# Kernel optimization log

Hardware: AMD Instinct MI355X
Metric: run time of the kernel (lower is better)

The kernel has to match this reference:

```python
import jax, jax.numpy as jnp
import numpy as np

D = 128      # internal_dimensions
L = 4        # num_edge_convs
N = 100000   # nodes
E = 800000   # edges
G = 64       # graphs
IN = 4       # in_channels


def _ln(x, g, b):
    m = jnp.mean(x, -1, keepdims=True)
    v = jnp.mean((x - m) ** 2, -1, keepdims=True)
    return (x - m) * jax.lax.rsqrt(v + 1e-5) * g + b


def _gelu(x):
    return jax.nn.gelu(x, approximate=False)  # torch nn.GELU default (erf)


def _seg_mean(x, seg, n):
    s = jax.ops.segment_sum(x, seg, num_segments=n)
    c = jax.ops.segment_sum(jnp.ones((x.shape[0], 1), x.dtype), seg, num_segments=n)
    return s / jnp.maximum(c, 1.0)


def _seg_max(x, seg, n):
    m = jax.ops.segment_max(x, seg, num_segments=n)
    return jnp.where(jnp.isfinite(m), m, 0.0)  # empty segments -> 0 (PyG convention)


def _forward(x, edge_index, batch, num_graphs,
             in_W1, in_b1, in_g1, in_bn1, in_W2, in_b2, in_g2, in_bn2,
             pre_g, pre_b, cW1, cb1, cg1, cbb1, cW2, cb2, cg2, cbb2, pW, pb,
             ag_g, ag_b,
             kW1, kb1, kg1, kbb1, kW2, kb2, kg2, kbb2,
             kW3, kb3, kg3, kbb3, kW4, kb4):
    n = x.shape[0]
    # input_net: Linear -> LN -> GELU -> Linear -> LN   (dropout=0, eval)
    h = _gelu(_ln(x @ in_W1 + in_b1, in_g1, in_bn1))
    h = _ln(h @ in_W2 + in_b2, in_g2, in_bn2)

    x_in_max = _seg_max(h, batch, num_graphs)
    x_in_mean = _seg_mean(h, batch, num_graphs)

    src, dst = edge_index[0], edge_index[1]  # PyG: message from src (x_j) to dst (x_i)
    xcur = h
    for l in range(L):
        identity = xcur
        hn = _ln(xcur, pre_g[l], pre_b[l])
        xi = hn[dst]            # [E, D]
        xj = hn[src]            # [E, D]
        m = jnp.concatenate([xi, xj - xi], axis=-1)       # [E, 2D]
        m = _gelu(_ln(m @ cW1[l] + cb1[l], cg1[l], cbb1[l]))
        m = _gelu(_ln(m @ cW2[l] + cb2[l], cg2[l], cbb2[l]))
        a_max = _seg_max(m, dst, n)
        a_mean = _seg_mean(m, dst, n)
        aggr = jnp.concatenate([a_max, a_mean], axis=-1)  # [N, 2D]
        xcur = identity + aggr @ pW[l] + pb[l]

    xcur = _ln(xcur, ag_g, ag_b)
    x_g_max = _seg_max(xcur, batch, num_graphs)
    x_g_mean = _seg_mean(xcur, batch, num_graphs)

    xp = jnp.concatenate([x_in_max, x_in_mean, x_g_max, x_g_mean], axis=-1)  # [G, 4D]
    z = _gelu(_ln(xp @ kW1 + kb1, kg1, kbb1))
    z = _gelu(_ln(z @ kW2 + kb2, kg2, kbb2))
    z = _gelu(_ln(z @ kW3 + kb3, kg3, kbb3))
    return z @ kW4 + kb4  # [G, 1]


def setup_inputs() -> dict:
    key = jax.random.key(0)
    ks = iter(jax.random.split(key, 64))
    def W(shape, fan):
        return jax.random.normal(next(ks), shape, jnp.float32) * np.float32((2.0 / fan) ** 0.5)
    inp = {}
    inp["x"] = jax.random.normal(next(ks), (N, IN), jnp.float32)
    inp["edge_index"] = jax.random.randint(next(ks), (2, E), 0, N)
    inp["batch"] = jnp.sort(jax.random.randint(next(ks), (N,), 0, G))
    inp["num_graphs"] = G
    inp["in_W1"] = W((IN, D), IN); inp["in_b1"] = jnp.zeros((D,), jnp.float32)
    inp["in_g1"] = jnp.ones((D,), jnp.float32); inp["in_bn1"] = jnp.zeros((D,), jnp.float32)
    inp["in_W2"] = W((D, D), D); inp["in_b2"] = jnp.zeros((D,), jnp.float32)
    inp["in_g2"] = jnp.ones((D,), jnp.float32); inp["in_bn2"] = jnp.zeros((D,), jnp.float32)
    inp["pre_g"] = jnp.ones((L, D), jnp.float32); inp["pre_b"] = jnp.zeros((L, D), jnp.float32)
    inp["cW1"] = W((L, 2 * D, D), 2 * D); inp["cb1"] = jnp.zeros((L, D), jnp.float32)
    inp["cg1"] = jnp.ones((L, D), jnp.float32); inp["cbb1"] = jnp.zeros((L, D), jnp.float32)
    inp["cW2"] = W((L, D, D), D); inp["cb2"] = jnp.zeros((L, D), jnp.float32)
    inp["cg2"] = jnp.ones((L, D), jnp.float32); inp["cbb2"] = jnp.zeros((L, D), jnp.float32)
    inp["pW"] = W((L, 2 * D, D), 2 * D); inp["pb"] = jnp.zeros((L, D), jnp.float32)
    inp["ag_g"] = jnp.ones((D,), jnp.float32); inp["ag_b"] = jnp.zeros((D,), jnp.float32)
    inp["kW1"] = W((4 * D, D), 4 * D); inp["kb1"] = jnp.zeros((D,), jnp.float32)
    inp["kg1"] = jnp.ones((D,), jnp.float32); inp["kbb1"] = jnp.zeros((D,), jnp.float32)
    inp["kW2"] = W((D, D), D); inp["kb2"] = jnp.zeros((D,), jnp.float32)
    inp["kg2"] = jnp.ones((D,), jnp.float32); inp["kbb2"] = jnp.zeros((D,), jnp.float32)
    inp["kW3"] = W((D, D // 4), D); inp["kb3"] = jnp.zeros((D // 4,), jnp.float32)
    inp["kg3"] = jnp.ones((D // 4,), jnp.float32); inp["kbb3"] = jnp.zeros((D // 4,), jnp.float32)
    inp["kW4"] = W((D // 4, 1), D // 4); inp["kb4"] = jnp.zeros((1,), jnp.float32)
    return inp


def reference(x, edge_index, batch, num_graphs,
              in_W1, in_b1, in_g1, in_bn1, in_W2, in_b2, in_g2, in_bn2,
              pre_g, pre_b, cW1, cb1, cg1, cbb1, cW2, cb2, cg2, cbb2, pW, pb,
              ag_g, ag_b,
              kW1, kb1, kg1, kbb1, kW2, kb2, kg2, kbb2,
              kW3, kb3, kg3, kbb3, kW4, kb4):
    return _forward(x, edge_index, batch, num_graphs,
                    in_W1, in_b1, in_g1, in_bn1, in_W2, in_b2, in_g2, in_bn2,
                    pre_g, pre_b, cW1, cb1, cg1, cbb1, cW2, cb2, cg2, cbb2, pW, pb,
                    ag_g, ag_b,
                    kW1, kb1, kg1, kbb1, kW2, kb2, kg2, kbb2,
                    kW3, kb3, kg3, kbb3, kW4, kb4)
```

## Files before the change

### kernel.cpp

```cpp
#include <hip/hip_runtime.h>
#include <hip/hip_bf16.h>
#include <math.h>

__device__ __forceinline__ float geluf(float x) {
    return 0.5f * x * (1.0f + erff(x * 0.70710678118654752f));
}
#define MAPNEGINF 0x007FFFFFu
__device__ __forceinline__ float funmap(unsigned m) {
    return __uint_as_float((m & 0x80000000u) ? (m ^ 0x80000000u) : ~m);
}
__device__ __forceinline__ unsigned fmap(float f) {
    unsigned u = __float_as_uint(f);
    return ((int)u < 0) ? ~u : (u | 0x80000000u);
}
__device__ __forceinline__ float wred64(float v) {
#pragma unroll
    for (int m = 1; m < 64; m <<= 1) v += __shfl_xor(v, m);
    return v;
}
__device__ __forceinline__ unsigned short bf16r(float f) {
    unsigned u = __float_as_uint(f);
    u += 0x7fffu + ((u >> 16) & 1u);
    return (unsigned short)(u >> 16);
}

__device__ __forceinline__ void stage_wq(float* Ws, const float* __restrict__ src, int t) {
#pragma unroll
    for (int it = 0; it < 4; ++it) {
        const int idx = it * 1024 + (t << 2);
        *(float4*)(Ws + idx) = *(const float4*)(src + idx);
    }
}

__device__ __forceinline__ void kloop_q(const float* As, const float* Ws, float (&acc)[4][8],
                                        const int r0, const int ogc, const int kb) {
#pragma unroll
    for (int kk = 0; kk < 32; kk += 4) {
        const float4 a0 = *(const float4*)(As + (r0 + 0) * 132 + kb + kk);
        const float4 a1 = *(const float4*)(As + (r0 + 1) * 132 + kb + kk);
        const float4 a2 = *(const float4*)(As + (r0 + 2) * 132 + kb + kk);
        const float4 a3 = *(const float4*)(As + (r0 + 3) * 132 + kb + kk);
#define MAD8(R, AV)                                                                     \
    {                                                                                   \
        acc[R][0] += (AV)*wA.x; acc[R][1] += (AV)*wA.y; acc[R][2] += (AV)*wA.z;         \
        acc[R][3] += (AV)*wA.w; acc[R][4] += (AV)*wB.x; acc[R][5] += (AV)*wB.y;         \
        acc[R][6] += (AV)*wB.z; acc[R][7] += (AV)*wB.w;                                 \
    }
#define KSTEP(J, C)                                                                     \
    {                                                                                   \
        const float4 wA = *(const float4*)(Ws + (kk + (J)) * 128 + ogc);                \
        const float4 wB = *(const float4*)(Ws + (kk + (J)) * 128 + 64 + ogc);           \
        MAD8(0, a0.C) MAD8(1, a1.C) MAD8(2, a2.C) MAD8(3, a3.C)                         \
    }
        KSTEP(0, x) KSTEP(1, y) KSTEP(2, z) KSTEP(3, w)
#undef KSTEP
#undef MAD8
    }
}

__global__ void k_zero(unsigned* __restrict__ p, int n) {
    const int i = blockIdx.x * 256 + threadIdx.x;
    if (i < n) p[i] = 0u;
}

__global__ void k_copyu(const unsigned* __restrict__ a, const unsigned* __restrict__ b,
                        unsigned* __restrict__ ac, unsigned* __restrict__ bc, int n) {
    const int i = blockIdx.x * 256 + threadIdx.x;
    if (i < n) {
        ac[i] = a[i];
        bc[i] = b[i];
    }
}

__global__ void k_count(const int* __restrict__ ei, unsigned* __restrict__ deg, int E) {
    const int e = blockIdx.x * 256 + threadIdx.x;
    if (e < E) atomicAdd(deg + ei[E + e], 1u);
}

__global__ void k_scan1(const unsigned* __restrict__ deg, unsigned* __restrict__ excl,
                        unsigned* __restrict__ bsum, int n) {
    __shared__ unsigned sh[256];
    const int t = threadIdx.x;
    const int base = blockIdx.x * 1024 + t * 4;
    unsigned v0 = (base + 0 < n) ? deg[base + 0] : 0u;
    unsigned v1 = (base + 1 < n) ? deg[base + 1] : 0u;
    unsigned v2 = (base + 2 < n) ? deg[base + 2] : 0u;
    unsigned v3 = (base + 3 < n) ? deg[base + 3] : 0u;
    const unsigned s = v0 + v1 + v2 + v3;
    sh[t] = s;
    __syncthreads();
    for (int off = 1; off < 256; off <<= 1) {
        unsigned x = 0;
        if (t >= off) x = sh[t - off];
        __syncthreads();
        if (t >= off) sh[t] += x;
        __syncthreads();
    }
    const unsigned ebase = sh[t] - s;
    if (base + 0 < n) excl[base + 0] = ebase;
    if (base + 1 < n) excl[base + 1] = ebase + v0;
    if (base + 2 < n) excl[base + 2] = ebase + v0 + v1;
    if (base + 3 < n) excl[base + 3] = ebase + v0 + v1 + v2;
    if (t == 255) bsum[blockIdx.x] = sh[255];
}

__global__ void k_scan2(unsigned* __restrict__ bsum, int nb) {
    __shared__ unsigned sh[256];
    const int t = threadIdx.x;
    const unsigned v = (t < nb) ? bsum[t] : 0u;
    sh[t] = v;
    __syncthreads();
    for (int off = 1; off < 256; off <<= 1) {
        unsigned x = 0;
        if (t >= off) x = sh[t - off];
        __syncthreads();
        if (t >= off) sh[t] += x;
        __syncthreads();
    }
    if (t < nb) bsum[t] = sh[t] - v;
}

__global__ void k_scan3(unsigned* __restrict__ excl, const unsigned* __restrict__ bsum, int n) {
    const int t = threadIdx.x;
    const int base = blockIdx.x * 1024 + t * 4;
    const unsigned add = bsum[blockIdx.x];
#pragma unroll
    for (int j = 0; j < 4; ++j)
        if (base + j < n) excl[base + j] += add;
}

__global__ void k_scatter(const int* __restrict__ ei, unsigned* __restrict__ cursor,
                          int* __restrict__ esrc, int* __restrict__ edst, int E) {
    const int e = blockIdx.x * 256 + threadIdx.x;
    if (e < E) {
        const int s = ei[e];
        const int d = ei[E + e];
        const unsigned pos = atomicAdd(cursor + d, 1u);
        esrc[pos] = s;
        edst[pos] = d;
    }
}

__global__ void k_in1(const float* __restrict__ x, const float* __restrict__ W1,
                      const float* __restrict__ b1, const float* __restrict__ g1,
                      const float* __restrict__ bn1, float* __restrict__ h, int n) {
    const int t = threadIdx.x, lane = t & 63, wave = t >> 6;
    const int d0 = lane << 1;
    const float2 w0 = *(const float2*)(W1 + d0);
    const float2 w1 = *(const float2*)(W1 + 128 + d0);
    const float2 w2 = *(const float2*)(W1 + 256 + d0);
    const float2 w3 = *(const float2*)(W1 + 384 + d0);
    const float2 bb = *(const float2*)(b1 + d0);
    const float2 gg = *(const float2*)(g1 + d0);
    const float2 nn = *(const float2*)(bn1 + d0);
    const int stride = gridDim.x * 4;
    for (int node = blockIdx.x * 4 + wave; node < n; node += stride) {
        const float4 xv = *(const float4*)(x + (size_t)node * 4);
        float h0 = bb.x + xv.x * w0.x + xv.y * w1.x + xv.z * w2.x + xv.w * w3.x;
        float h1 = bb.y + xv.x * w0.y + xv.y * w1.y + xv.z * w2.y + xv.w * w3.y;
        const float s = wred64(h0 + h1), q = wred64(h0 * h0 + h1 * h1);
        const float mean = s * 0.0078125f, var = q * 0.0078125f - mean * mean;
        const float rs = rsqrtf(var + 1e-5f);
        h0 = geluf((h0 - mean) * rs * gg.x + nn.x);
        h1 = geluf((h1 - mean) * rs * gg.y + nn.y);
        *(float2*)(h + (size_t)node * 128 + d0) = make_float2(h0, h1);
    }
}

__global__ __launch_bounds__(256, 2) void k_in2(const float* __restrict__ A,
                                                const float* __restrict__ W,
                                                const float* __restrict__ bias,
                                                const float* __restrict__ g,
                                                const float* __restrict__ b,
                                                float* __restrict__ C, int n) {
    __shared__ float As[64 * 132];
    __shared__ float Ws[4096];
    const int t = threadIdx.x;
    const int n0 = blockIdx.x * 64;
    {
        const int r = t >> 2, c0 = (t & 3) << 5;
        const int row = n0 + r;
        const bool ok = row < n;
#pragma unroll
        for (int j = 0; j < 8; ++j) {
            const int col = c0 + (j << 2);
            float4 v = make_float4(0.f, 0.f, 0.f, 0.f);
            if (ok) v = *(const float4*)(A + (size_t)row * 128 + col);
            *(float4*)(As + r * 132 + col) = v;
        }
    }
    float acc[4][8];
#pragma unroll
    for (int r = 0; r < 4; ++r)
#pragma unroll
        for (int o = 0; o < 8; ++o) acc[r][o] = 0.f;
    const int og = t & 15, eg = t >> 4;
    const int ogc = og << 2, r0 = eg << 2;
#pragma unroll
    for (int q4 = 0; q4 < 4; ++q4) {
        stage_wq(Ws, W + q4 * 4096, t);
        __syncthreads();
        kloop_q(As, Ws, acc, r0, ogc, q4 * 32);
        __syncthreads();
    }
    const float4 bA = *(const float4*)(bias + ogc);
    const float4 bB = *(const float4*)(bias + 64 + ogc);
    const float4 gA = *(const float4*)(g + ogc);
    const float4 gB = *(const float4*)(g + 64 + ogc);
    const float4 lA = *(const float4*)(b + ogc);
    const float4 lB = *(const float4*)(b + 64 + ogc);
#pragma unroll
    for (int r = 0; r < 4; ++r) {
        float v[8];
        v[0] = acc[r][0] + bA.x; v[1] = acc[r][1] + bA.y;
        v[2] = acc[r][2] + bA.z; v[3] = acc[r][3] + bA.w;
        v[4] = acc[r][4] + bB.x; v[5] = acc[r][5] + bB.y;
        v[6] = acc[r][6] + bB.z; v[7] = acc[r][7] + bB.w;
        float s = 0.f, q = 0.f;
#pragma unroll
        for (int o = 0; o < 8; ++o) { s += v[o]; q += v[o] * v[o]; }
#pragma unroll
        for (int m = 1; m < 16; m <<= 1) { s += __shfl_xor(s, m); q += __shfl_xor(q, m); }
        const float mean = s * 0.0078125f;
        const float var = q * 0.0078125f - mean * mean;
        const float rs = rsqrtf(var + 1e-5f);
        const int row = n0 + r0 + r;
        if (row < n) {
            *(float4*)(C + (size_t)row * 128 + ogc) = make_float4(
                (v[0] - mean) * rs * gA.x + lA.x, (v[1] - mean) * rs * gA.y + lA.y,
                (v[2] - mean) * rs * gA.z + lA.z, (v[3] - mean) * rs * gA.w + lA.w);
            *(float4*)(C + (size_t)row * 128 + 64 + ogc) = make_float4(
                (v[4] - mean) * rs * gB.x + lB.x, (v[5] - mean) * rs * gB.y + lB.y,
                (v[6] - mean) * rs * gB.z + lB.z, (v[7] - mean) * rs * gB.w + lB.w);
        }
    }
}

__global__ void k_ln(const float* __restrict__ in, const float* __restrict__ g,
                     const float* __restrict__ b, float* __restrict__ out, int n) {
    const int t = threadIdx.x, lane = t & 63, wave = t >> 6;
    const int d0 = lane << 1;
    const float ga = g[d0], gb = g[d0 + 1], ba = b[d0], bb = b[d0 + 1];
    const int stride = gridDim.x * 4;
    for (int node = blockIdx.x * 4 + wave; node < n; node += stride) {
        const float2 v = *(const float2*)(in + (size_t)node * 128 + d0);
        const float s = wred64(v.x + v.y), q = wred64(v.x * v.x + v.y * v.y);
        const float mean = s * 0.0078125f, var = q * 0.0078125f - mean * mean;
        const float rs = rsqrtf(var + 1e-5f);
        *(float2*)(out + (size_t)node * 128 + d0) =
            make_float2((v.x - mean) * rs * ga + ba, (v.y - mean) * rs * gb + bb);
    }
}

__global__ void k_wxj(const float* __restrict__ c, float* __restrict__ Wx,
                      float* __restrict__ Wj) {
    const int idx = blockIdx.x * 256 + threadIdx.x;
    const float a = c[idx], b = c[16384 + idx];
    Wx[idx] = a - b;
    Wj[idx] = b;
}

__global__ __launch_bounds__(256, 2) void k_gemmh(const float* __restrict__ A,
                                                  const float* __restrict__ W,
                                                  const float* __restrict__ bias,
                                                  unsigned short* __restrict__ C, int n) {
    __shared__ float As[64 * 132];
    __shared__ float Ws[4096];
    const int t = threadIdx.x;
    const int n0 = blockIdx.x * 64;
    {
        const int r = t >> 2, c0 = (t & 3) << 5;
        const int row = n0 + r;
        const bool ok = row < n;
#pragma unroll
        for (int j = 0; j < 8; ++j) {
            const int col = c0 + (j << 2);
            float4 v = make_float4(0.f, 0.f, 0.f, 0.f);
            if (ok) v = *(const float4*)(A + (size_t)row * 128 + col);
            *(float4*)(As + r * 132 + col) = v;
        }
    }
    float acc[4][8];
#pragma unroll
    for (int r = 0; r < 4; ++r)
#pragma unroll
        for (int o = 0; o < 8; ++o) acc[r][o] = 0.f;
    const int og = t & 15, eg = t >> 4;
    const int ogc = og << 2, r0 = eg << 2;
#pragma unroll
    for (int q4 = 0; q4 < 4; ++q4) {
        stage_wq(Ws, W + q4 * 4096, t);
        __syncthreads();
        kloop_q(As, Ws, acc, r0, ogc, q4 * 32);
        __syncthreads();
    }
    float4 bA = make_float4(0.f, 0.f, 0.f, 0.f), bB = bA;
    if (bias) {
        bA = *(const float4*)(bias + ogc);
        bB = *(const float4*)(bias + 64 + ogc);
    }
#pragma unroll
    for (int r = 0; r < 4; ++r) {
        const int row = n0 + r0 + r;
        if (row < n) {
            ushort4 u0, u1;
            u0.x = bf16r(acc[r][0] + bA.x); u0.y = bf16r(acc[r][1] + bA.y);
            u0.z = bf16r(acc[r][2] + bA.z); u0.w = bf16r(acc[r][3] + bA.w);
            u1.x = bf16r(acc[r][4] + bB.x); u1.y = bf16r(acc[r][5] + bB.y);
            u1.z = bf16r(acc[r][6] + bB.z); u1.w = bf16r(acc[r][7] + bB.w);
            *(ushort4*)(C + (size_t)row * 128 + ogc) = u0;
            *(ushort4*)(C + (size_t)row * 128 + 64 + ogc) = u1;
        }
    }
}

__global__ void k_gather(const unsigned short* __restrict__ P,
                         const unsigned short* __restrict__ Q, const int* __restrict__ esrc,
                         const int* __restrict__ edst, const float* __restrict__ g1,
                         const float* __restrict__ b1, float* __restrict__ U, int e0, int e1) {
    const int t = threadIdx.x, lane = t & 63, wave = t >> 6;
    const int d0 = lane << 1;
    const float ga = g1[d0], gb = g1[d0 + 1], ba = b1[d0], bb = b1[d0 + 1];
    const int stride = gridDim.x * 4;
    for (int e = e0 + blockIdx.x * 4 + wave; e < e1; e += stride) {
        const int s = esrc[e], d = edst[e];
        const unsigned pu = *(const unsigned*)(P + ((size_t)d << 7) + d0);
        const unsigned qu = *(const unsigned*)(Q + ((size_t)s << 7) + d0);
        const float x0 = __uint_as_float(pu << 16) + __uint_as_float(qu << 16);
        const float x1 = __uint_as_float(pu & 0xffff0000u) + __uint_as_float(qu & 0xffff0000u);
        const float su = wred64(x0 + x1);
        const float qq = wred64(x0 * x0 + x1 * x1);
        const float mean = su * 0.0078125f;
        const float var = qq * 0.0078125f - mean * mean;
        const float rs = rsqrtf(var + 1e-5f);
        *(float2*)(U + (size_t)(e - e0) * 128 + d0) = make_float2(
            geluf((x0 - mean) * rs * ga + ba), geluf((x1 - mean) * rs * gb + bb));
    }
}

__global__ __launch_bounds__(256, 2) void k_gemme(
    const float* __restrict__ U, const int* __restrict__ edst, const float* __restrict__ W2,
    const float* __restrict__ cb2, const float* __restrict__ g2, const float* __restrict__ b2,
    const unsigned* __restrict__ rowend, const unsigned* __restrict__ degc,
    float* __restrict__ amax, float* __restrict__ asum, float* __restrict__ recmax,
    float* __restrict__ recsum, int* __restrict__ recid, int e0, int E) {
    __shared__ float Us[64 * 132];
    __shared__ float Ws[4096];
    __shared__ int sdst[64];
    __shared__ float scb2[128], sg2[128], sb2[128];
    const int t = threadIdx.x;
    const int base = e0 + blockIdx.x * 64;
    if (base >= E) return;
    const int gb = base >> 6;
    if (t < 64) {
        const int idx = base + t;
        sdst[t] = (idx < E) ? edst[idx] : -1;
    }
    if (t >= 128) {
        const int d = t - 128;
        scb2[d] = cb2[d];
        sg2[d] = g2[d];
        sb2[d] = b2[d];
    }
    {
        const int r = t >> 2, c0 = (t & 3) << 5;
        const bool ok = (base + r) < E;
        const float* src = U + (size_t)(base - e0 + r) * 128;
#pragma unroll
        for (int j = 0; j < 8; ++j) {
            const int col = c0 + (j << 2);
            float4 v = make_float4(0.f, 0.f, 0.f, 0.f);
            if (ok) v = *(const float4*)(src + col);
            *(float4*)(Us + r * 132 + col) = v;
        }
    }
    float acc[4][8];
#pragma unroll
    for (int r = 0; r < 4; ++r)
#pragma unroll
        for (int o = 0; o < 8; ++o) acc[r][o] = 0.f;
    const int og = t & 15, eg = t >> 4;
    const int ogc = og << 2, r0 = eg << 2;
#pragma unroll
    for (int q4 = 0; q4 < 4; ++q4) {
        stage_wq(Ws, W2 + q4 * 4096, t);
        __syncthreads();
        kloop_q(Us, Ws, acc, r0, ogc, q4 * 32);
        __syncthreads();
    }
#pragma unroll
    for (int r = 0; r < 4; ++r) {
        float v[8];
        float s = 0.f, q = 0.f;
#pragma unroll
        for (int o = 0; o < 8; ++o) {
            const int col = (o < 4) ? (ogc + o) : (64 + ogc + o - 4);
            v[o] = acc[r][o] + scb2[col];
            s += v[o];
            q += v[o] * v[o];
        }
#pragma unroll
        for (int m = 1; m < 16; m <<= 1) { s += __shfl_xor(s, m); q += __shfl_xor(q, m); }
        const float mean = s * 0.0078125f;
        const float var = q * 0.0078125f - mean * mean;
        const float rs = rsqrtf(var + 1e-5f);
#pragma unroll
        for (int o = 0; o < 8; ++o) {
            const int col = (o < 4) ? (ogc + o) : (64 + ogc + o - 4);
            v[o] = geluf((v[o] - mean) * rs * sg2[col] + sb2[col]);
        }
        *(float4*)(Us + (r0 + r) * 132 + ogc) = make_float4(v[0], v[1], v[2], v[3]);
        *(float4*)(Us + (r0 + r) * 132 + 64 + ogc) = make_float4(v[4], v[5], v[6], v[7]);
    }
    __syncthreads();
    if (t < 128) {
        int cur = sdst[0], istart = 0;
        float vmax = -INFINITY, vsum = 0.f;
        int id0 = -1, id1 = -1;
        auto flush = [&](int iend) {
            const unsigned re = rowend[cur];
            const unsigned rs0 = re - degc[cur];
            const unsigned ps = (unsigned)(base + istart), pe = (unsigned)(base + iend);
            if (ps == rs0 && pe == re) {
                amax[(size_t)cur * 128 + t] = vmax;
                asum[(size_t)cur * 128 + t] = vsum;
            } else {
                const int slot = (istart == 0) ? 0 : 1;
                const size_t ro = (size_t)(2 * gb + slot) * 128 + t;
                recmax[ro] = vmax;
                recsum[ro] = vsum;
                if (slot == 0) id0 = cur; else id1 = cur;
            }
        };
        for (int i = 0; i < 64; ++i) {
            const int dn = sdst[i];
            if (dn != cur) {
                if (cur >= 0) flush(i);
                cur = dn;
                istart = i;
                vmax = -INFINITY;
                vsum = 0.f;
            }
            if (dn >= 0) {
                const float v = Us[i * 132 + t];
                vmax = fmaxf(vmax, v);
                vsum += v;
            }
        }
        if (cur >= 0) flush(64);
        if (t == 0) {
            recid[2 * gb] = id0;
            recid[2 * gb + 1] = id1;
        }
    }
}

__global__ void k_merge(const unsigned* __restrict__ rowend, const unsigned* __restrict__ degc,
                        const float* __restrict__ recmax, const float* __restrict__ recsum,
                        const int* __restrict__ recid, float* __restrict__ amax,
                        float* __restrict__ asum, int n) {
    const int node = blockIdx.x * 2 + (threadIdx.x >> 7);
    const int t = threadIdx.x & 127;
    if (node >= n) return;
    const unsigned dg = degc[node];
    if (dg == 0u) {
        amax[(size_t)node * 128 + t] = 0.f;
        asum[(size_t)node * 128 + t] = 0.f;
        return;
    }
    const unsigned re = rowend[node], rs = re - dg;
    const int b0 = rs >> 6, b1 = (re - 1) >> 6;
    if (b0 == b1) return;
    float m = -INFINITY, s = 0.f;
    for (int b = b0; b <= b1; ++b) {
#pragma unroll
        for (int sl = 0; sl < 2; ++sl) {
            if (recid[2 * b + sl] == node) {
                const size_t ro = (size_t)(2 * b + sl) * 128 + t;
                m = fmaxf(m, recmax[ro]);
                s += recsum[ro];
            }
        }
    }
    amax[(size_t)node * 128 + t] = m;
    asum[(size_t)node * 128 + t] = s;
}

__global__ void k_mean(float* __restrict__ asum, const unsigned* __restrict__ degc, int n32) {
    for (int i = blockIdx.x * 256 + threadIdx.x; i < n32; i += gridDim.x * 256) {
        const int row = i >> 5;
        const unsigned dv = degc[row];
        const float inv = 1.f / (float)(dv < 1u ? 1u : dv);
        float4 v = ((float4*)asum)[i];
        ((float4*)asum)[i] = make_float4(v.x * inv, v.y * inv, v.z * inv, v.w * inv);
    }
}

__global__ __launch_bounds__(256, 2) void k_update(const float* __restrict__ amax,
                                                   const float* __restrict__ amean,
                                                   const float* __restrict__ pW,
                                                   const float* __restrict__ pb,
                                                   float* __restrict__ xcur, int n) {
    __shared__ float As[64 * 132];
    __shared__ float Ws[4096];
    const int t = threadIdx.x;
    const int n0 = blockIdx.x * 64;
    const int og = t & 15, eg = t >> 4;
    const int ogc = og << 2, r0 = eg << 2;
    float acc[4][8];
#pragma unroll
    for (int r = 0; r < 4; ++r)
#pragma unroll
        for (int o = 0; o < 8; ++o) acc[r][o] = 0.f;
    const int r = t >> 2, c0 = (t & 3) << 5;
    const int row = n0 + r;
    const bool ok = row < n;
#pragma unroll
    for (int pass = 0; pass < 2; ++pass) {
        const float* src = (pass == 0) ? amax : amean;
#pragma unroll
        for (int j = 0; j < 8; ++j) {
            const int col = c0 + (j << 2);
            float4 v = make_float4(0.f, 0.f, 0.f, 0.f);
            if (ok) v = *(const float4*)(src + (size_t)row * 128 + col);
            *(float4*)(As + r * 132 + col) = v;
        }
#pragma unroll
        for (int q4 = 0; q4 < 4; ++q4) {
            stage_wq(Ws, pW + (size_t)(pass * 128 + q4 * 32) * 128, t);
            __syncthreads();
            kloop_q(As, Ws, acc, r0, ogc, q4 * 32);
            __syncthreads();
        }
    }
    const float4 bA = *(const float4*)(pb + ogc);
    const float4 bB = *(const float4*)(pb + 64 + ogc);
#pragma unroll
    for (int rr = 0; rr < 4; ++rr) {
        const int orow = n0 + r0 + rr;
        if (orow < n) {
            const float4 x0 = *(const float4*)(xcur + (size_t)orow * 128 + ogc);
            const float4 x1 = *(const float4*)(xcur + (size_t)orow * 128 + 64 + ogc);
            *(float4*)(xcur + (size_t)orow * 128 + ogc) =
                make_float4(x0.x + acc[rr][0] + bA.x, x0.y + acc[rr][1] + bA.y,
                            x0.z + acc[rr][2] + bA.z, x0.w + acc[rr][3] + bA.w);
            *(float4*)(xcur + (size_t)orow * 128 + 64 + ogc) =
                make_float4(x1.x + acc[rr][4] + bB.x, x1.y + acc[rr][5] + bB.y,
                            x1.z + acc[rr][6] + bB.z, x1.w + acc[rr][7] + bB.w);
        }
    }
}

__global__ void k_pool_init(unsigned* __restrict__ gmax1, float* __restrict__ gsum1,
                            unsigned* __restrict__ gcount1, unsigned* __restrict__ gmax2,
                            float* __restrict__ gsum2, unsigned* __restrict__ gcount2, int ng) {
    const int i = blockIdx.x * 256 + threadIdx.x;
    if (i < ng * 128) {
        gmax1[i] = MAPNEGINF;
        gsum1[i] = 0.f;
        gmax2[i] = MAPNEGINF;
        gsum2[i] = 0.f;
    }
    if (i < ng) {
        gcount1[i] = 0u;
        gcount2[i] = 0u;
    }
}

__global__ void k_pool(const float* __restrict__ in, const int* __restrict__ batch,
                       unsigned* __restrict__ gmax, float* __restrict__ gsum,
                       unsigned* __restrict__ gcount, int n) {
    const int t = threadIdx.x;
    if (t >= 128) return;
    const int per = (n + gridDim.x - 1) / gridDim.x;
    const int i0 = blockIdx.x * per;
    const int i1 = min(n, i0 + per);
    if (i0 >= i1) return;
    int cur = batch[i0];
    float vmax = -INFINITY, vsum = 0.f;
    unsigned cnt = 0;
    for (int i = i0; i < i1; ++i) {
        const int g = batch[i];
        if (g != cur) {
            atomicMax(gmax + (size_t)cur * 128 + t, fmap(vmax));
            atomicAdd(gsum + (size_t)cur * 128 + t, vsum);
            if (t == 0) atomicAdd(gcount + cur, cnt);
            cur = g;
            vmax = -INFINITY;
            vsum = 0.f;
            cnt = 0;
        }
        const float v = in[(size_t)i * 128 + t];
        vmax = fmaxf(vmax, v);
        vsum += v;
        cnt++;
    }
    atomicMax(gmax + (size_t)cur * 128 + t, fmap(vmax));
    atomicAdd(gsum + (size_t)cur * 128 + t, vsum);
    if (t == 0) atomicAdd(gcount + cur, cnt);
}

__global__ void k_xp(const unsigned* __restrict__ gmax1, const float* __restrict__ gsum1,
                     const unsigned* __restrict__ gcount1, const unsigned* __restrict__ gmax2,
                     const float* __restrict__ gsum2, const unsigned* __restrict__ gcount2,
                     float* __restrict__ xp) {
    const int g = blockIdx.x, d = threadIdx.x;
    const unsigned c1u = gcount1[g], c2u = gcount2[g];
    const float c1 = (float)(c1u < 1u ? 1u : c1u);
    const float c2 = (float)(c2u < 1u ? 1u : c2u);
    const unsigned m1 = gmax1[g * 128 + d], m2 = gmax2[g * 128 + d];
    xp[g * 512 + d] = (m1 == MAPNEGINF) ? 0.f : funmap(m1);
    xp[g * 512 + 128 + d] = gsum1[g * 128 + d] / c1;
    xp[g * 512 + 256 + d] = (m2 == MAPNEGINF) ? 0.f : funmap(m2);
    xp[g * 512 + 384 + d] = gsum2[g * 128 + d] / c2;
}

__global__ __launch_bounds__(64) void k_know(
    const float* __restrict__ xp, const float* __restrict__ kW1, const float* __restrict__ kb1,
    const float* __restrict__ kg1, const float* __restrict__ kbb1, const float* __restrict__ kW2,
    const float* __restrict__ kb2, const float* __restrict__ kg2, const float* __restrict__ kbb2,
    const float* __restrict__ kW3, const float* __restrict__ kb3, const float* __restrict__ kg3,
    const float* __restrict__ kbb3, const float* __restrict__ kW4, const float* __restrict__ kb4,
    float* __restrict__ out) {
    __shared__ float sh[512];
    __shared__ float s3[32];
    const int l = threadIdx.x, g = blockIdx.x;
    const int d0 = l << 1;
    *(float4*)(sh + l * 8) = *(const float4*)(xp + g * 512 + l * 8);
    *(float4*)(sh + l * 8 + 4) = *(const float4*)(xp + g * 512 + l * 8 + 4);
    __syncthreads();
    float a0 = kb1[d0], a1 = kb1[d0 + 1];
    for (int k = 0; k < 512; ++k) {
        const float u = sh[k];
        const float2 w = *(const float2*)(kW1 + k * 128 + d0);
        a0 += u * w.x;
        a1 += u * w.y;
    }
    {
        const float s = wred64(a0 + a1), q = wred64(a0 * a0 + a1 * a1);
        const float mean = s * 0.0078125f, var = q * 0.0078125f - mean * mean;
        const float rs = rsqrtf(var + 1e-5f);
        a0 = geluf((a0 - mean) * rs * kg1[d0] + kbb1[d0]);
        a1 = geluf((a1 - mean) * rs * kg1[d0 + 1] + kbb1[d0 + 1]);
    }
    __syncthreads();
    sh[d0] = a0;
    sh[d0 + 1] = a1;
    __syncthreads();
    float b0v = kb2[d0], b1v = kb2[d0 + 1];
    for (int k = 0; k < 128; ++k) {
        const float u = sh[k];
        const float2 w = *(const float2*)(kW2 + k * 128 + d0);
        b0v += u * w.x;
        b1v += u * w.y;
    }
    {
        const float s = wred64(b0v + b1v), q = wred64(b0v * b0v + b1v * b1v);
        const float mean = s * 0.0078125f, var = q * 0.0078125f - mean * mean;
        const float rs = rsqrtf(var + 1e-5f);
        b0v = geluf((b0v - mean) * rs * kg2[d0] + kbb2[d0]);
        b1v = geluf((b1v - mean) * rs * kg2[d0 + 1] + kbb2[d0 + 1]);
    }
    __syncthreads();
    sh[d0] = b0v;
    sh[d0 + 1] = b1v;
    __syncthreads();
    const int d3 = (l & 15) << 1;
    float c0 = kb3[d3], c1 = kb3[d3 + 1];
    for (int k = 0; k < 128; ++k) {
        const float u = sh[k];
        const float2 w = *(const float2*)(kW3 + k * 32 + d3);
        c0 += u * w.x;
        c1 += u * w.y;
    }
    {
        float s = c0 + c1, q = c0 * c0 + c1 * c1;
#pragma unroll
        for (int m = 1; m < 16; m <<= 1) {
            s += __shfl_xor(s, m);
            q += __shfl_xor(q, m);
        }
        const float mean = s * 0.03125f, var = q * 0.03125f - mean * mean;
        const float rs = rsqrtf(var + 1e-5f);
        c0 = geluf((c0 - mean) * rs * kg3[d3] + kbb3[d3]);
        c1 = geluf((c1 - mean) * rs * kg3[d3 + 1] + kbb3[d3 + 1]);
    }
    if (l < 16) {
        s3[d3] = c0;
        s3[d3 + 1] = c1;
    }
    __syncthreads();
    if (l == 0) {
        float rr = kb4[0];
        for (int k = 0; k < 32; ++k) rr += s3[k] * kW4[k];
        out[g] = rr;
    }
}

extern "C" void kernel_launch(void* const* d_in, const int* in_sizes, int n_in, void* d_out,
                              int out_size, void* d_ws, size_t ws_size, hipStream_t stream) {
    const int N = in_sizes[0] / 4;
    const int E = in_sizes[1] / 2;
    const int G = 64;
    const int L = 4;

    const float* x = (const float*)d_in[0];
    const int* ei = (const int*)d_in[1];
    const int* batch = (const int*)d_in[2];
    const float* inW1 = (const float*)d_in[4];
    const float* inb1 = (const float*)d_in[5];
    const float* ing1 = (const float*)d_in[6];
    const float* inbn1 = (const float*)d_in[7];
    const float* inW2 = (const float*)d_in[8];
    const float* inb2 = (const float*)d_in[9];
    const float* ing2 = (const float*)d_in[10];
    const float* inbn2 = (const float*)d_in[11];
    const float* pre_g = (const float*)d_in[12];
    const float* pre_b = (const float*)d_in[13];
    const float* cW1 = (const float*)d_in[14];
    const float* cb1 = (const float*)d_in[15];
    const float* cg1 = (const float*)d_in[16];
    const float* cbb1 = (const float*)d_in[17];
    const float* cW2 = (const float*)d_in[18];
    const float* cb2 = (const float*)d_in[19];
    const float* cg2 = (const float*)d_in[20];
    const float* cbb2 = (const float*)d_in[21];
    const float* pW = (const float*)d_in[22];
    const float* pb = (const float*)d_in[23];
    const float* ag_g = (const float*)d_in[24];
    const float* ag_b = (const float*)d_in[25];
    const float* kW1 = (const float*)d_in[26];
    const float* kb1 = (const float*)d_in[27];
    const float* kg1 = (const float*)d_in[28];
    const float* kbb1 = (const float*)d_in[29];
    const float* kW2 = (const float*)d_in[30];
    const float* kb2 = (const float*)d_in[31];
    const float* kg2 = (const float*)d_in[32];
    const float* kbb2 = (const float*)d_in[33];
    const float* kW3 = (const float*)d_in[34];
    const float* kb3 = (const float*)d_in[35];
    const float* kg3 = (const float*)d_in[36];
    const float* kbb3 = (const float*)d_in[37];
    const float* kW4 = (const float*)d_in[38];
    const float* kb4 = (const float*)d_in[39];
    float* out = (float*)d_out;

    const int CHUNK_BLOCKS = 782;
    const int CHUNK_E = CHUNK_BLOCKS * 64;
    const int nblk64 = (E + 63) / 64;
    const int nchunks = (nblk64 + CHUNK_BLOCKS - 1) / CHUNK_BLOCKS;

    char* wsb = (char*)d_ws;
    size_t off = 0;
    auto ALC = [&](size_t bytes) {
        void* p = wsb + off;
        off = (off + bytes + 255) & ~(size_t)255;
        return p;
    };
    const size_t NB = (size_t)N * 128 * 4;
    float* xcur = (float*)ALC(NB);
    float* hn = (float*)ALC(NB);
    float* amax = hn;
    float* asum = (float*)ALC(NB);
    unsigned short* Pb = (unsigned short*)ALC((size_t)N * 128 * 2);
    unsigned short* Qb = (unsigned short*)ALC((size_t)N * 128 * 2);
    float* U = (float*)ALC((size_t)CHUNK_E * 128 * 4);
    unsigned* deg = (unsigned*)ALC((size_t)N * 4);
    unsigned* cursor = (unsigned*)ALC((size_t)N * 4);
    unsigned* degc = (unsigned*)ALC((size_t)N * 4);
    unsigned* rowend = (unsigned*)ALC((size_t)N * 4);
    unsigned* bsum = (unsigned*)ALC(4096);
    int* esrc = (int*)ALC((size_t)E * 4);
    int* edst = (int*)ALC((size_t)E * 4);
    float* recmax = (float*)ALC((size_t)nblk64 * 2 * 128 * 4);
    float* recsum = (float*)ALC((size_t)nblk64 * 2 * 128 * 4);
    int* recid = (int*)ALC((size_t)nblk64 * 2 * 4);
    float* Wx = (float*)ALC(65536);
    float* Wj = (float*)ALC(65536);
    unsigned* gmax1 = (unsigned*)ALC((size_t)G * 128 * 4);
    float* gsum1 = (float*)ALC((size_t)G * 128 * 4);
    unsigned* gcount1 = (unsigned*)ALC((size_t)G * 4);
    unsigned* gmax2 = (unsigned*)ALC((size_t)G * 128 * 4);
    float* gsum2 = (float*)ALC((size_t)G * 128 * 4);
    unsigned* gcount2 = (unsigned*)ALC((size_t)G * 4);
    float* xp = (float*)ALC((size_t)G * 512 * 4);

    if (off > ws_size) {
        k_zero<<<(out_size + 255) / 256, 256, 0, stream>>>((unsigned*)d_out, out_size);
        return;
    }

    k_zero<<<(N + 255) / 256, 256, 0, stream>>>(deg, N);
    k_count<<<(E + 255) / 256, 256, 0, stream>>>(ei, deg, E);
    const int nb = (N + 1023) / 1024;
    k_scan1<<<nb, 256, 0, stream>>>(deg, cursor, bsum, N);
    k_scan2<<<1, 256, 0, stream>>>(bsum, nb);
    k_scan3<<<nb, 256, 0, stream>>>(cursor, bsum, N);
    k_scatter<<<(E + 255) / 256, 256, 0, stream>>>(ei, cursor, esrc, edst, E);
    k_copyu<<<(N + 255) / 256, 256, 0, stream>>>(deg, cursor, degc, rowend, N);

    const int gemmGrid = (N + 63) / 64;
    k_in1<<<1024, 256, 0, stream>>>(x, inW1, inb1, ing1, inbn1, hn, N);
    k_in2<<<gemmGrid, 256, 0, stream>>>(hn, inW2, inb2, ing2, inbn2, xcur, N);
    k_pool_init<<<(G * 128 + 255) / 256, 256, 0, stream>>>(gmax1, gsum1, gcount1, gmax2, gsum2,
                                                           gcount2, G);
    k_pool<<<512, 256, 0, stream>>>(xcur, batch, gmax1, gsum1, gcount1, N);

    for (int l = 0; l < L; ++l) {
        k_wxj<<<64, 256, 0, stream>>>(cW1 + (size_t)l * 32768, Wx, Wj);
        k_ln<<<1024, 256, 0, stream>>>(xcur, pre_g + l * 128, pre_b + l * 128, hn, N);
        k_gemmh<<<gemmGrid, 256, 0, stream>>>(hn, Wx, cb1 + l * 128, Pb, N);
        k_gemmh<<<gemmGrid, 256, 0, stream>>>(hn, Wj, (const float*)nullptr, Qb, N);
        for (int c = 0; c < nchunks; ++c) {
            const int e0 = c * CHUNK_E;
            const int e1 = min(E, e0 + CHUNK_E);
            if (e0 >= E) break;
            k_gather<<<2048, 256, 0, stream>>>(Pb, Qb, esrc, edst, cg1 + l * 128, cbb1 + l * 128,
                                               U, e0, e1);
            k_gemme<<<CHUNK_BLOCKS, 256, 0, stream>>>(
                U, edst, cW2 + (size_t)l * 16384, cb2 + l * 128, cg2 + l * 128, cbb2 + l * 128,
                rowend, degc, amax, asum, recmax, recsum, recid, e0, E);
        }
        k_merge<<<(N + 1) / 2, 256, 0, stream>>>(rowend, degc, recmax, recsum, recid, amax, asum,
                                                 N);
        k_mean<<<2048, 256, 0, stream>>>(asum, degc, N * 32);
        k_update<<<gemmGrid, 256, 0, stream>>>(amax, asum, pW + (size_t)l * 32768, pb + l * 128,
                                               xcur, N);
    }

    k_ln<<<1024, 256, 0, stream>>>(xcur, ag_g, ag_b, hn, N);
    k_pool<<<512, 256, 0, stream>>>(hn, batch, gmax2, gsum2, gcount2, N);
    k_xp<<<G, 128, 0, stream>>>(gmax1, gsum1, gcount1, gmax2, gsum2, gcount2, xp);
    k_know<<<G, 64, 0, stream>>>(xp, kW1, kb1, kg1, kbb1, kW2, kb2, kg2, kbb2, kW3, kb3, kg3,
                                 kbb3, kW4, kb4, out);
}
```

Measured before the change: 97.47 ms.

## Fuse pre-LayerNorm into node GEMMs, fold mean into update, halve GEMM tiles

The per-layer LayerNorm kernel is removed and its normalization now runs inside k_gemmh while the A tile is staged. The separate mean-division kernel is removed and the division by degree happens while k_update loads its A tile. The node GEMM tiles shrink from 64 to 32 rows with launch bounds raised to 4 blocks per CU. This saves several full N×128 memory passes and kernel launches, but the LayerNorm is now computed twice (once per gemmh call) and the smaller tiles reuse staged weights less.

After: 103.0 ms. +5.6%, slower.

```diff
diff --git a/kernel.cpp b/kernel.cpp
--- a/kernel.cpp
+++ b/kernel.cpp
@@ -51,6 +51,30 @@
         const float4 wA = *(const float4*)(Ws + (kk + (J)) * 128 + ogc);                \
         const float4 wB = *(const float4*)(Ws + (kk + (J)) * 128 + 64 + ogc);           \
         MAD8(0, a0.C) MAD8(1, a1.C) MAD8(2, a2.C) MAD8(3, a3.C)                         \
+    }
+        KSTEP(0, x) KSTEP(1, y) KSTEP(2, z) KSTEP(3, w)
+#undef KSTEP
+#undef MAD8
+    }
+}
+
+__device__ __forceinline__ void kloop2(const float* As, const float* Ws, float (&acc)[2][8],
+                                       const int r0, const int ogc, const int kb) {
+#pragma unroll
+    for (int kk = 0; kk < 32; kk += 4) {
+        const float4 a0 = *(const float4*)(As + (r0 + 0) * 132 + kb + kk);
+        const float4 a1 = *(const float4*)(As + (r0 + 1) * 132 + kb + kk);
+#define MAD8(R, AV)                                                                     \
+    {                                                                                   \
+        acc[R][0] += (AV)*wA.x; acc[R][1] += (AV)*wA.y; acc[R][2] += (AV)*wA.z;         \
+        acc[R][3] += (AV)*wA.w; acc[R][4] += (AV)*wB.x; acc[R][5] += (AV)*wB.y;         \
+        acc[R][6] += (AV)*wB.z; acc[R][7] += (AV)*wB.w;                                 \
+    }
+#define KSTEP(J, C)                                                                     \
+    {                                                                                   \
+        const float4 wA = *(const float4*)(Ws + (kk + (J)) * 128 + ogc);                \
+        const float4 wB = *(const float4*)(Ws + (kk + (J)) * 128 + 64 + ogc);           \
+        MAD8(0, a0.C) MAD8(1, a1.C)                                                     \
     }
         KSTEP(0, x) KSTEP(1, y) KSTEP(2, z) KSTEP(3, w)
 #undef KSTEP
@@ -167,40 +191,40 @@
     }
 }
 
-__global__ __launch_bounds__(256, 2) void k_in2(const float* __restrict__ A,
+__global__ __launch_bounds__(256, 4) void k_in2(const float* __restrict__ A,
                                                 const float* __restrict__ W,
                                                 const float* __restrict__ bias,
                                                 const float* __restrict__ g,
                                                 const float* __restrict__ b,
                                                 float* __restrict__ C, int n) {
-    __shared__ float As[64 * 132];
+    __shared__ float As[32 * 132];
     __shared__ float Ws[4096];
     const int t = threadIdx.x;
-    const int n0 = blockIdx.x * 64;
+    const int n0 = blockIdx.x * 32;
     {
-        const int r = t >> 2, c0 = (t & 3) << 5;
+        const int r = t >> 3, c0 = (t & 7) << 4;
         const int row = n0 + r;
         const bool ok = row < n;
 #pragma unroll
-        for (int j = 0; j < 8; ++j) {
+        for (int j = 0; j < 4; ++j) {
             const int col = c0 + (j << 2);
             float4 v = make_float4(0.f, 0.f, 0.f, 0.f);
             if (ok) v = *(const float4*)(A + (size_t)row * 128 + col);
             *(float4*)(As + r * 132 + col) = v;
         }
     }
-    float acc[4][8];
-#pragma unroll
-    for (int r = 0; r < 4; ++r)
+    float acc[2][8];
+#pragma unroll
+    for (int r = 0; r < 2; ++r)
 #pragma unroll
         for (int o = 0; o < 8; ++o) acc[r][o] = 0.f;
     const int og = t & 15, eg = t >> 4;
-    const int ogc = og << 2, r0 = eg << 2;
+    const int ogc = og << 2, r0 = eg << 1;
 #pragma unroll
     for (int q4 = 0; q4 < 4; ++q4) {
         stage_wq(Ws, W + q4 * 4096, t);
         __syncthreads();
-        kloop_q(As, Ws, acc, r0, ogc, q4 * 32);
+        kloop2(As, Ws, acc, r0, ogc, q4 * 32);
         __syncthreads();
     }
     const float4 bA = *(const float4*)(bias + ogc);
@@ -210,7 +234,7 @@
     const float4 lA = *(const float4*)(b + ogc);
     const float4 lB = *(const float4*)(b + 64 + ogc);
 #pragma unroll
-    for (int r = 0; r < 4; ++r) {
+    for (int r = 0; r < 2; ++r) {
         float v[8];
         v[0] = acc[r][0] + bA.x; v[1] = acc[r][1] + bA.y;
         v[2] = acc[r][2] + bA.z; v[3] = acc[r][3] + bA.w;
@@ -260,38 +284,63 @@
     Wj[idx] = b;
 }
 
-__global__ __launch_bounds__(256, 2) void k_gemmh(const float* __restrict__ A,
+__global__ __launch_bounds__(256, 4) void k_gemmh(const float* __restrict__ A,
+                                                  const float* __restrict__ g,
+                                                  const float* __restrict__ b,
                                                   const float* __restrict__ W,
                                                   const float* __restrict__ bias,
                                                   unsigned short* __restrict__ C, int n) {
-    __shared__ float As[64 * 132];
+    __shared__ float As[32 * 132];
     __shared__ float Ws[4096];
+    __shared__ float sg[128], sb[128];
     const int t = threadIdx.x;
-    const int n0 = blockIdx.x * 64;
+    const int n0 = blockIdx.x * 32;
+    if (t < 128) { sg[t] = g[t]; sb[t] = b[t]; }
+    __syncthreads();
     {
-        const int r = t >> 2, c0 = (t & 3) << 5;
+        const int r = t >> 3, c0 = (t & 7) << 4;
         const int row = n0 + r;
         const bool ok = row < n;
-#pragma unroll
-        for (int j = 0; j < 8; ++j) {
-            const int col = c0 + (j << 2);
-            float4 v = make_float4(0.f, 0.f, 0.f, 0.f);
-            if (ok) v = *(const float4*)(A + (size_t)row * 128 + col);
-            *(float4*)(As + r * 132 + col) = v;
-        }
-    }
-    float acc[4][8];
-#pragma unroll
-    for (int r = 0; r < 4; ++r)
+        float4 v4[4];
+        float s = 0.f, q = 0.f;
+        if (ok) {
+#pragma unroll
+            for (int j = 0; j < 4; ++j) {
+                v4[j] = *(const float4*)(A + (size_t)row * 128 + c0 + (j << 2));
+                s += v4[j].x + v4[j].y + v4[j].z + v4[j].w;
+                q += v4[j].x * v4[j].x + v4[j].y * v4[j].y + v4[j].z * v4[j].z +
+                     v4[j].w * v4[j].w;
+            }
+        } else {
+#pragma unroll
+            for (int j = 0; j < 4; ++j) v4[j] = make_float4(0.f, 0.f, 0.f, 0.f);
+        }
+        s += __shfl_xor(s, 1); s += __shfl_xor(s, 2); s += __shfl_xor(s, 4);
+        q += __shfl_xor(q, 1); q += __shfl_xor(q, 2); q += __shfl_xor(q, 4);
+        const float mean = s * 0.0078125f;
+        const float var = q * 0.0078125f - mean * mean;
+        const float rs = rsqrtf(var + 1e-5f);
+#pragma unroll
+        for (int j = 0; j < 4; ++j) {
+            const int c = c0 + (j << 2);
+            As[r * 132 + c + 0] = (v4[j].x - mean) * rs * sg[c + 0] + sb[c + 0];
+            As[r * 132 + c + 1] = (v4[j].y - mean) * rs * sg[c + 1] + sb[c + 1];
+            As[r * 132 + c + 2] = (v4[j].z - mean) * rs * sg[c + 2] + sb[c + 2];
+            As[r * 132 + c + 3] = (v4[j].w - mean) * rs * sg[c + 3] + sb[c + 3];
+        }
+    }
+    float acc[2][8];
+#pragma unroll
+    for (int r = 0; r < 2; ++r)
 #pragma unroll
         for (int o = 0; o < 8; ++o) acc[r][o] = 0.f;
     const int og = t & 15, eg = t >> 4;
-    const int ogc = og << 2, r0 = eg << 2;
+    const int ogc = og << 2, r0 = eg << 1;
 #pragma unroll
     for (int q4 = 0; q4 < 4; ++q4) {
         stage_wq(Ws, W + q4 * 4096, t);
         __syncthreads();
-        kloop_q(As, Ws, acc, r0, ogc, q4 * 32);
+        kloop2(As, Ws, acc, r0, ogc, q4 * 32);
         __syncthreads();
     }
     float4 bA = make_float4(0.f, 0.f, 0.f, 0.f), bB = bA;
@@ -300,7 +349,7 @@
         bB = *(const float4*)(bias + 64 + ogc);
     }
 #pragma unroll
-    for (int r = 0; r < 4; ++r) {
+    for (int r = 0; r < 2; ++r) {
         const int row = n0 + r0 + r;
         if (row < n) {
             ushort4 u0, u1;
@@ -486,57 +535,65 @@
     asum[(size_t)node * 128 + t] = s;
 }
 
-__global__ void k_mean(float* __restrict__ asum, const unsigned* __restrict__ degc, int n32) {
-    for (int i = blockIdx.x * 256 + threadIdx.x; i < n32; i += gridDim.x * 256) {
-        const int row = i >> 5;
-        const unsigned dv = degc[row];
-        const float inv = 1.f / (float)(dv < 1u ? 1u : dv);
-        float4 v = ((float4*)asum)[i];
-        ((float4*)asum)[i] = make_float4(v.x * inv, v.y * inv, v.z * inv, v.w * inv);
-    }
-}
-
-__global__ __launch_bounds__(256, 2) void k_update(const float* __restrict__ amax,
-                                                   const float* __restrict__ amean,
+__global__ __launch_bounds__(256, 4) void k_update(const float* __restrict__ amax,
+                                                   const float* __restrict__ asum,
+                                                   const unsigned* __restrict__ degc,
                                                    const float* __restrict__ pW,
                                                    const float* __restrict__ pb,
                                                    float* __restrict__ xcur, int n) {
-    __shared__ float As[64 * 132];
+    __shared__ float As[32 * 132];
     __shared__ float Ws[4096];
     const int t = threadIdx.x;
-    const int n0 = blockIdx.x * 64;
+    const int n0 = blockIdx.x * 32;
     const int og = t & 15, eg = t >> 4;
-    const int ogc = og << 2, r0 = eg << 2;
-    float acc[4][8];
-#pragma unroll
-    for (int r = 0; r < 4; ++r)
+    const int ogc = og << 2, r0 = eg << 1;
+    float acc[2][8];
+#pragma unroll
+    for (int r = 0; r < 2; ++r)
 #pragma unroll
         for (int o = 0; o < 8; ++o) acc[r][o] = 0.f;
-    const int r = t >> 2, c0 = (t & 3) << 5;
+    const int r = t >> 3, c0 = (t & 7) << 4;
     const int row = n0 + r;
     const bool ok = row < n;
 #pragma unroll
     for (int pass = 0; pass < 2; ++pass) {
-        const float* src = (pass == 0) ? amax : amean;
-#pragma unroll
-        for (int j = 0; j < 8; ++j) {
-            const int col = c0 + (j << 2);
-            float4 v = make_float4(0.f, 0.f, 0.f, 0.f);
-            if (ok) v = *(const float4*)(src + (size_t)row * 128 + col);
-            *(float4*)(As + r * 132 + col) = v;
+        if (pass == 0) {
+#pragma unroll
+            for (int j = 0; j < 4; ++j) {
+                const int col = c0 + (j << 2);
+                float4 v = make_float4(0.f, 0.f, 0.f, 0.f);
+                if (ok) v = *(const float4*)(amax + (size_t)row * 128 + col);
+                *(float4*)(As + r * 132 + col) = v;
+            }
+        } else {
+            float inv = 0.f;
+            if (ok) {
+                const unsigned dv = degc[row];
+                inv = 1.f / (float)(dv < 1u ? 1u : dv);
+            }
+#pragma unroll
+            for (int j = 0; j < 4; ++j) {
+                const int col = c0 + (j << 2);
+                float4 v = make_float4(0.f, 0.f, 0.f, 0.f);
+                if (ok) {
+                    const float4 sv = *(const float4*)(asum + (size_t)row * 128 + col);
+                    v = make_float4(sv.x * inv, sv.y * inv, sv.z * inv, sv.w * inv);
+                }
+                *(float4*)(As + r * 132 + col) = v;
+            }
         }
 #pragma unroll
         for (int q4 = 0; q4 < 4; ++q4) {
             stage_wq(Ws, pW + (size_t)(pass * 128 + q4 * 32) * 128, t);
             __syncthreads();
-            kloop_q(As, Ws, acc, r0, ogc, q4 * 32);
+            kloop2(As, Ws, acc, r0, ogc, q4 * 32);
             __syncthreads();
         }
     }
     const float4 bA = *(const float4*)(pb + ogc);
     const float4 bB = *(const float4*)(pb + 64 + ogc);
 #pragma unroll
-    for (int rr = 0; rr < 4; ++rr) {
+    for (int rr = 0; rr < 2; ++rr) {
         const int orow = n0 + r0 + rr;
         if (orow < n) {
             const float4 x0 = *(const float4*)(xcur + (size_t)orow * 128 + ogc);
@@ -759,8 +816,7 @@
     };
     const size_t NB = (size_t)N * 128 * 4;
     float* xcur = (float*)ALC(NB);
-    float* hn = (float*)ALC(NB);
-    float* amax = hn;
+    float* amax = (float*)ALC(NB);
     float* asum = (float*)ALC(NB);
     unsigned short* Pb = (unsigned short*)ALC((size_t)N * 128 * 2);
     unsigned short* Qb = (unsigned short*)ALC((size_t)N * 128 * 2);
@@ -799,18 +855,19 @@
     k_scatter<<<(E + 255) / 256, 256, 0, stream>>>(ei, cursor, esrc, edst, E);
     k_copyu<<<(N + 255) / 256, 256, 0, stream>>>(deg, cursor, degc, rowend, N);
 
-    const int gemmGrid = (N + 63) / 64;
-    k_in1<<<1024, 256, 0, stream>>>(x, inW1, inb1, ing1, inbn1, hn, N);
-    k_in2<<<gemmGrid, 256, 0, stream>>>(hn, inW2, inb2, ing2, inbn2, xcur, N);
+    const int grid32 = (N + 31) / 32;
+    k_in1<<<1024, 256, 0, stream>>>(x, inW1, inb1, ing1, inbn1, amax, N);
+    k_in2<<<grid32, 256, 0, stream>>>(amax, inW2, inb2, ing2, inbn2, xcur, N);
     k_pool_init<<<(G * 128 + 255) / 256, 256, 0, stream>>>(gmax1, gsum1, gcount1, gmax2, gsum2,
                                                            gcount2, G);
     k_pool<<<512, 256, 0, stream>>>(xcur, batch, gmax1, gsum1, gcount1, N);
 
     for (int l = 0; l < L; ++l) {
         k_wxj<<<64, 256, 0, stream>>>(cW1 + (size_t)l * 32768, Wx, Wj);
-        k_ln<<<1024, 256, 0, stream>>>(xcur, pre_g + l * 128, pre_b + l * 128, hn, N);
-        k_gemmh<<<gemmGrid, 256, 0, stream>>>(hn, Wx, cb1 + l * 128, Pb, N);
-        k_gemmh<<<gemmGrid, 256, 0, stream>>>(hn, Wj, (const float*)nullptr, Qb, N);
+        k_gemmh<<<grid32, 256, 0, stream>>>(xcur, pre_g + l * 128, pre_b + l * 128, Wx,
+                                            cb1 + l * 128, Pb, N);
+        k_gemmh<<<grid32, 256, 0, stream>>>(xcur, pre_g + l * 128, pre_b + l * 128, Wj,
+                                            (const float*)nullptr, Qb, N);
         for (int c = 0; c < nchunks; ++c) {
             const int e0 = c * CHUNK_E;
             const int e1 = min(E, e0 + CHUNK_E);
@@ -823,13 +880,12 @@
         }
         k_merge<<<(N + 1) / 2, 256, 0, stream>>>(rowend, degc, recmax, recsum, recid, amax, asum,
                                                  N);
-        k_mean<<<2048, 256, 0, stream>>>(asum, degc, N * 32);
-        k_update<<<gemmGrid, 256, 0, stream>>>(amax, asum, pW + (size_t)l * 32768, pb + l * 128,
-                                               xcur, N);
-    }
-
-    k_ln<<<1024, 256, 0, stream>>>(xcur, ag_g, ag_b, hn, N);
-    k_pool<<<512, 256, 0, stream>>>(hn, batch, gmax2, gsum2, gcount2, N);
+        k_update<<<grid32, 256, 0, stream>>>(amax, asum, degc, pW + (size_t)l * 32768,
+                                             pb + l * 128, xcur, N);
+    }
+
+    k_ln<<<1024, 256, 0, stream>>>(xcur, ag_g, ag_b, amax, N);
+    k_pool<<<512, 256, 0, stream>>>(amax, batch, gmax2, gsum2, gcount2, N);
     k_xp<<<G, 128, 0, stream>>>(gmax1, gsum1, gcount1, gmax2, gsum2, gcount2, xp);
     k_know<<<G, 64, 0, stream>>>(xp, kW1, kb1, kg1, kbb1, kW2, kb2, kg2, kbb2, kW3, kb3, kg3,
                                  kbb3, kW4, kb4, out);
```
